# Kernel tuning notes

Measured on AMD Instinct MI355X. Metric: run time of the kernel, lower is better.

The kernel has to match this reference:

```python
import jax, jax.numpy as jnp
import numpy as np

DIM = 1024
HEADS = 16
DIM_HEAD = 64
INNER = HEADS * DIM_HEAD  # 1024
EPS = 1e-5


def setup_inputs() -> dict:
    key = jax.random.key(0)
    ks = jax.random.split(key, 8)
    B, N = 4, 2048
    s = 0.02
    return {
        "query": jax.random.normal(ks[0], (B, N, DIM), jnp.float32),
        "key_": jax.random.normal(ks[1], (B, N, DIM), jnp.float32),
        "value": jax.random.normal(ks[2], (B, N, DIM), jnp.float32),
        "Wq": jax.random.normal(ks[3], (DIM, INNER), jnp.float32) * s,
        "Wk": jax.random.normal(ks[4], (DIM, INNER), jnp.float32) * s,
        "Wv": jax.random.normal(ks[5], (DIM, INNER), jnp.float32) * s,
        "Wo": jax.random.normal(ks[6], (INNER, DIM), jnp.float32) * s,
        "bo": jnp.zeros((DIM,), jnp.float32),
        "gamma": jnp.ones((DIM,), jnp.float32),
        "beta": jnp.zeros((DIM,), jnp.float32),
    }


def reference(query, key_, value, Wq, Wk, Wv, Wo, bo, gamma, beta):
    B, N, _ = query.shape
    scale = DIM_HEAD ** (-0.5)
    # project and split heads: [B, H, N, Dh]
    q = (query @ Wq).reshape(B, N, HEADS, DIM_HEAD).transpose(0, 2, 1, 3)
    k = (key_ @ Wk).reshape(B, N, HEADS, DIM_HEAD).transpose(0, 2, 1, 3)
    v = (value @ Wv).reshape(B, N, HEADS, DIM_HEAD).transpose(0, 2, 1, 3)
    dots = jnp.einsum("bhnd,bhmd->bhnm", q, k) * scale  # [B,H,N,N]
    attn = jax.nn.softmax(dots, axis=-1)
    out = jnp.einsum("bhnm,bhmd->bhnd", attn, v)
    out = out.transpose(0, 2, 1, 3).reshape(B, N, INNER)
    out = out @ Wo + bo  # dropout p=0.0 is identity
    # LayerNorm over last dim
    mu = out.mean(-1, keepdims=True)
    var = ((out - mu) ** 2).mean(-1, keepdims=True)
    normed = (out - mu) * jax.lax.rsqrt(var + EPS) * gamma + beta
    return normed + query
```

## Files before the change

### kernel.cpp

```cpp
#include <hip/hip_runtime.h>
#include <stdint.h>

#define K_DIM 1024
#define B_SZ 4
#define N_SEQ 2048
#define HEADS 16
#define DH 64
#define M_TOT (B_SZ * N_SEQ)

typedef __bf16 bf16x8 __attribute__((ext_vector_type(8)));
typedef __bf16 bf16x4 __attribute__((ext_vector_type(4)));
typedef __bf16 bf16x2 __attribute__((ext_vector_type(2)));
typedef float f32x4 __attribute__((ext_vector_type(4)));
typedef float f32x16 __attribute__((ext_vector_type(16)));

typedef const uint32_t __attribute__((address_space(1))) gas_u32;
typedef uint32_t __attribute__((address_space(3))) las_u32;

#define CE_SCALE 0.1803368801f

__device__ __forceinline__ uint16_t f2bf(float f) {
  uint32_t u = __float_as_uint(f);
  u += 0x7FFFu + ((u >> 16) & 1u);
  return (uint16_t)(u >> 16);
}

__device__ __forceinline__ void gld_lds16(const uint16_t* g, uint16_t* lds) {
  __builtin_amdgcn_global_load_lds((gas_u32*)g, (las_u32*)lds, 16, 0, 0);
}

__device__ __forceinline__ uint32_t pkbf(float a, float b) {
  bf16x2 t;
  t[0] = (__bf16)a;
  t[1] = (__bf16)b;
  return __builtin_bit_cast(uint32_t, t);
}

__device__ __forceinline__ void pswap(uint32_t& a, uint32_t& b) {
  asm("v_permlane32_swap_b32 %0, %1" : "+v"(a), "+v"(b));
}

__global__ __launch_bounds__(256) void conv_bf16_k(const float* __restrict__ s0,
                                                   const float* __restrict__ s1,
                                                   const float* __restrict__ s2,
                                                   uint16_t* __restrict__ dstbase, int n4) {
  const int z = blockIdx.y;
  const float* src = (z == 0) ? s0 : (z == 1) ? s1 : s2;
  uint16_t* dst = dstbase + (size_t)z * M_TOT * K_DIM;
  int i = blockIdx.x * blockDim.x + threadIdx.x;
  if (i < n4) {
    float4 v = ((const float4*)src)[i];
    ushort4 o;
    o.x = f2bf(v.x); o.y = f2bf(v.y); o.z = f2bf(v.z); o.w = f2bf(v.w);
    ((ushort4*)dst)[i] = o;
  }
}

__global__ __launch_bounds__(256) void transpose_conv(const float* __restrict__ s0,
                                                      const float* __restrict__ s1,
                                                      const float* __restrict__ s2,
                                                      const float* __restrict__ s3,
                                                      uint16_t* __restrict__ dstbase) {
  __shared__ float tile[32][33];
  const int z = blockIdx.z;
  const float* src = (z == 0) ? s0 : (z == 1) ? s1 : (z == 2) ? s2 : s3;
  uint16_t* dst = dstbase + (size_t)z * 1024 * 1024;
  const int tx = threadIdx.x, ty = threadIdx.y;
  const int bx = blockIdx.x * 32, by = blockIdx.y * 32;
#pragma unroll
  for (int i = 0; i < 32; i += 8)
    tile[ty + i][tx] = src[(size_t)(by + ty + i) * 1024 + bx + tx];
  __syncthreads();
#pragma unroll
  for (int i = 0; i < 32; i += 8)
    dst[(size_t)(bx + ty + i) * 1024 + by + tx] = f2bf(tile[tx][ty + i]);
}

template <int MODE>
__global__ __launch_bounds__(256, 2) void gemm_bf16(const uint16_t* __restrict__ A,
                                                    const uint16_t* __restrict__ BT,
                                                    void* __restrict__ Cout,
                                                    const float* __restrict__ bias) {
  __shared__ __align__(16) uint16_t As[2][128 * 32];
  __shared__ __align__(16) uint16_t Bs[2][128 * 32];
  const int tid = threadIdx.x;
  const int wave = tid >> 6, lane = tid & 63;
  const int g = lane >> 4, c16 = lane & 15;

  const int bid = blockIdx.x;
  const int xcd = bid & 7;
  const int l = bid >> 3;
  const int z = (MODE == 3) ? (l >> 6) : 0;
  const int r = l & 63;
  const int n0 = (r & 7) * 128;
  const int m0 = (xcd * 8 + (r >> 3)) * 128;

  const int wr = wave >> 1, wc = wave & 1;
  float scale = 1.f;
  if (MODE == 3) {
    A += (size_t)z * M_TOT * K_DIM;
    BT += (size_t)z * 1024 * 1024;
    scale = (z == 0) ? CE_SCALE : 1.f;
  }

  const f32x4 fzero = {0.f, 0.f, 0.f, 0.f};
  f32x4 acc[4][4];
#pragma unroll
  for (int i = 0; i < 4; ++i)
#pragma unroll
    for (int j = 0; j < 4; ++j) acc[i][j] = fzero;

  const int srow = wave * 32 + (lane >> 2);
  const int scol = (((lane & 3) ^ ((srow >> 1) & 3)) * 8);
  const uint16_t* ag0 = A + (size_t)(m0 + srow) * K_DIM + scol;
  const uint16_t* ag1 = A + (size_t)(m0 + srow + 16) * K_DIM + scol;
  const uint16_t* bg0 = BT + (size_t)(n0 + srow) * K_DIM + scol;
  const uint16_t* bg1 = BT + (size_t)(n0 + srow + 16) * K_DIM + scol;
  const int lofa0 = (wave * 32) * 32;
  const int lofa1 = (wave * 32 + 16) * 32;

  const int rk = (c16 >> 1) & 3;

  gld_lds16(ag0, &As[0][lofa0]);
  gld_lds16(ag1, &As[0][lofa1]);
  gld_lds16(bg0, &Bs[0][lofa0]);
  gld_lds16(bg1, &Bs[0][lofa1]);
  __syncthreads();

  int cur = 0;
  for (int kt = 0; kt < K_DIM / 32; ++kt) {
    if (kt + 1 < K_DIM / 32) {
      const int nxt = cur ^ 1;
      gld_lds16(ag0 + (kt + 1) * 32, &As[nxt][lofa0]);
      gld_lds16(ag1 + (kt + 1) * 32, &As[nxt][lofa1]);
      gld_lds16(bg0 + (kt + 1) * 32, &Bs[nxt][lofa0]);
      gld_lds16(bg1 + (kt + 1) * 32, &Bs[nxt][lofa1]);
    }
    bf16x8 avec[4], bvec[4];
#pragma unroll
    for (int i = 0; i < 4; ++i)
      avec[i] = *(const bf16x8*)&As[cur][(wr * 64 + i * 16 + c16) * 32 + ((g ^ rk) << 3)];
#pragma unroll
    for (int j = 0; j < 4; ++j)
      bvec[j] = *(const bf16x8*)&Bs[cur][(wc * 64 + j * 16 + c16) * 32 + ((g ^ rk) << 3)];
#pragma unroll
    for (int i = 0; i < 4; ++i)
#pragma unroll
      for (int j = 0; j < 4; ++j)
        acc[i][j] = __builtin_amdgcn_mfma_f32_16x16x32_bf16(avec[i], bvec[j], acc[i][j], 0, 0, 0);
    __syncthreads();
    cur ^= 1;
  }

#pragma unroll
  for (int i = 0; i < 4; ++i) {
#pragma unroll
    for (int j = 0; j < 4; ++j) {
      const int col = n0 + wc * 64 + j * 16 + c16;
      if (MODE == 3 && z == 2) {
        const int h = col >> 6, d = col & 63;
        const int row0 = m0 + wr * 64 + i * 16 + g * 4;
        const int b = row0 >> 11, n = row0 & 2047;
        ushort4 o;
        o.x = f2bf(acc[i][j][0]); o.y = f2bf(acc[i][j][1]);
        o.z = f2bf(acc[i][j][2]); o.w = f2bf(acc[i][j][3]);
        *(ushort4*)&((uint16_t*)Cout)[(size_t)2 * M_TOT * 1024 +
                                      (((size_t)(b * HEADS + h)) * DH + d) * N_SEQ + n] = o;
      } else {
#pragma unroll
        for (int r2 = 0; r2 < 4; ++r2) {
          const int row = m0 + wr * 64 + i * 16 + g * 4 + r2;
          if (MODE == 3) {
            const int b = row >> 11, n = row & 2047;
            const int h = col >> 6, d = col & 63;
            ((uint16_t*)Cout)[(size_t)z * M_TOT * 1024 +
                              (((size_t)(b * HEADS + h)) * N_SEQ + n) * DH + d] =
                f2bf(acc[i][j][r2] * scale);
          } else {
            ((float*)Cout)[(size_t)row * 1024 + col] = acc[i][j][r2] + bias[col];
          }
        }
      }
    }
  }
}

__global__ __launch_bounds__(256, 2) void attention_k(const uint16_t* __restrict__ qm,
                                                      const uint16_t* __restrict__ km,
                                                      const uint16_t* __restrict__ vtm,
                                                      uint16_t* __restrict__ om) {
  __shared__ __align__(16) uint16_t Ks[2 * 64 * 64];
  __shared__ __align__(16) uint16_t Vs[2 * 64 * 64];
  const int tid = threadIdx.x;
  const int wave = tid >> 6, lane = tid & 63;
  const int lrow = lane & 31;
  const int hi = lane >> 5;

  const int bid = blockIdx.x;
  const int xcd = bid & 7;
  const int l0 = bid >> 3;
  const int bh = xcd * 8 + (l0 & 7);
  const int qblk = l0 >> 3;
  const int b = bh >> 4, h = bh & 15;
  const int q0w = qblk * 256 + wave * 64;

  const uint16_t* qbase = qm + (size_t)bh * N_SEQ * DH;
  const uint16_t* kbase = km + (size_t)bh * N_SEQ * DH;
  const uint16_t* vbase = vtm + (size_t)bh * DH * N_SEQ;

  bf16x8 qf[2][4];
#pragma unroll
  for (int qs = 0; qs < 2; ++qs) {
    const uint16_t* qp = qbase + (size_t)(q0w + qs * 32 + lrow) * DH + hi * 8;
#pragma unroll
    for (int step = 0; step < 4; ++step) qf[qs][step] = *(const bf16x8*)(qp + step * 16);
  }

  int koff[2][4];
  int voff[2][2][2];
#pragma unroll
  for (int ks = 0; ks < 2; ++ks) {
    const int krow = ks * 32 + lrow;
#pragma unroll
    for (int step = 0; step < 4; ++step)
      koff[ks][step] = krow * 64 + ((((step << 1) | hi) ^ (krow & 7)) << 3);
#pragma unroll
    for (int s = 0; s < 2; ++s)
#pragma unroll
      for (int dt = 0; dt < 2; ++dt)
        voff[ks][s][dt] =
            (dt * 32 + lrow) * 64 + ((((ks << 2) | (s << 1) | hi) ^ (lrow & 7)) << 3);
  }

  f32x16 oacc[2][2];
#pragma unroll
  for (int qs = 0; qs < 2; ++qs)
#pragma unroll
    for (int dt = 0; dt < 2; ++dt)
#pragma unroll
      for (int i = 0; i < 16; ++i) oacc[qs][dt][i] = 0.f;
  float l[2] = {0.f, 0.f};

  const int ch = tid & 7;
  const int krow0 = tid >> 3, krow1 = 32 + (tid >> 3);
  const int kdst0 = krow0 * 64 + ((ch ^ (krow0 & 7)) << 3);
  const int kdst1 = krow1 * 64 + ((ch ^ (krow1 & 7)) << 3);

  uint4 kp0, kp1, vp0, vp1;
  kp0 = *(const uint4*)&kbase[(size_t)tid * 8];
  kp1 = *(const uint4*)&kbase[(size_t)(256 + tid) * 8];
  vp0 = *(const uint4*)&vbase[(size_t)krow0 * N_SEQ + ch * 8];
  vp1 = *(const uint4*)&vbase[(size_t)krow1 * N_SEQ + ch * 8];
  *(uint4*)&Ks[kdst0] = kp0;
  *(uint4*)&Ks[kdst1] = kp1;
  *(uint4*)&Vs[kdst0] = vp0;
  *(uint4*)&Vs[kdst1] = vp1;
  __syncthreads();

  for (int t = 0; t < N_SEQ / 64; ++t) {
    const int cur = t & 1;
    if (t < N_SEQ / 64 - 1) {
      const size_t ko = (size_t)(t + 1) * 4096;
      const int vc = (t + 1) * 64;
      kp0 = *(const uint4*)&kbase[ko + (size_t)tid * 8];
      kp1 = *(const uint4*)&kbase[ko + (size_t)(256 + tid) * 8];
      vp0 = *(const uint4*)&vbase[(size_t)krow0 * N_SEQ + vc + ch * 8];
      vp1 = *(const uint4*)&vbase[(size_t)krow1 * N_SEQ + vc + ch * 8];
    }
    const uint16_t* ksp = &Ks[cur * 4096];
    const uint16_t* vsp = &Vs[cur * 4096];

#pragma unroll
    for (int ks = 0; ks < 2; ++ks) {
      bf16x8 kf[4];
#pragma unroll
      for (int step = 0; step < 4; ++step) kf[step] = *(const bf16x8*)&ksp[koff[ks][step]];

      f32x16 z[2];
#pragma unroll
      for (int qs = 0; qs < 2; ++qs)
#pragma unroll
        for (int i = 0; i < 16; ++i) z[qs][i] = 0.f;

      __builtin_amdgcn_s_setprio(1);
#pragma unroll
      for (int step = 0; step < 4; ++step)
        z[0] = __builtin_amdgcn_mfma_f32_32x32x16_bf16(kf[step], qf[0][step], z[0], 0, 0, 0);
#pragma unroll
      for (int step = 0; step < 4; ++step)
        z[1] = __builtin_amdgcn_mfma_f32_32x32x16_bf16(kf[step], qf[1][step], z[1], 0, 0, 0);
      __builtin_amdgcn_s_setprio(0);

      uint32_t pa[2][2][4];
#pragma unroll
      for (int qs = 0; qs < 2; ++qs) {
        float p[16];
#pragma unroll
        for (int r = 0; r < 16; ++r) p[r] = __builtin_amdgcn_exp2f(z[qs][r]);
        l[qs] += (((p[0] + p[1]) + (p[2] + p[3])) + ((p[4] + p[5]) + (p[6] + p[7]))) +
                 (((p[8] + p[9]) + (p[10] + p[11])) + ((p[12] + p[13]) + (p[14] + p[15])));
#pragma unroll
        for (int s = 0; s < 2; ++s) {
          uint32_t w0 = pkbf(p[s * 8 + 0], p[s * 8 + 1]);
          uint32_t w1 = pkbf(p[s * 8 + 2], p[s * 8 + 3]);
          uint32_t w2 = pkbf(p[s * 8 + 4], p[s * 8 + 5]);
          uint32_t w3 = pkbf(p[s * 8 + 6], p[s * 8 + 7]);
          pswap(w0, w2);
          pswap(w1, w3);
          pa[qs][s][0] = w0; pa[qs][s][1] = w1; pa[qs][s][2] = w2; pa[qs][s][3] = w3;
        }
      }

      bf16x8 vf[2][2];
#pragma unroll
      for (int s = 0; s < 2; ++s)
#pragma unroll
        for (int dt = 0; dt < 2; ++dt) vf[s][dt] = *(const bf16x8*)&vsp[voff[ks][s][dt]];

      __builtin_amdgcn_s_setprio(1);
#pragma unroll
      for (int s = 0; s < 2; ++s)
#pragma unroll
        for (int qs = 0; qs < 2; ++qs) {
          uint4 u;
          u.x = pa[qs][s][0]; u.y = pa[qs][s][1]; u.z = pa[qs][s][2]; u.w = pa[qs][s][3];
          const bf16x8 paf = __builtin_bit_cast(bf16x8, u);
          oacc[qs][0] = __builtin_amdgcn_mfma_f32_32x32x16_bf16(paf, vf[s][0], oacc[qs][0], 0, 0, 0);
          oacc[qs][1] = __builtin_amdgcn_mfma_f32_32x32x16_bf16(paf, vf[s][1], oacc[qs][1], 0, 0, 0);
        }
      __builtin_amdgcn_s_setprio(0);
    }

    if (t < N_SEQ / 64 - 1) {
      *(uint4*)&Ks[(cur ^ 1) * 4096 + kdst0] = kp0;
      *(uint4*)&Ks[(cur ^ 1) * 4096 + kdst1] = kp1;
      *(uint4*)&Vs[(cur ^ 1) * 4096 + kdst0] = vp0;
      *(uint4*)&Vs[(cur ^ 1) * 4096 + kdst1] = vp1;
      __syncthreads();
    }
  }

#pragma unroll
  for (int qs = 0; qs < 2; ++qs) l[qs] += __shfl_xor(l[qs], 32);

#pragma unroll
  for (int qs = 0; qs < 2; ++qs) {
#pragma unroll
    for (int r = 0; r < 16; ++r) {
      const int ql = (r & 3) + 8 * (r >> 2) + 4 * hi;
      const float lr = __shfl(l[qs], ql);
      const float inv = 1.f / lr;
      const int row = q0w + qs * 32 + ql;
      const size_t base = ((size_t)b * N_SEQ + row) * 1024 + h * 64;
      om[base + lrow] = f2bf(oacc[qs][0][r] * inv);
      om[base + 32 + lrow] = f2bf(oacc[qs][1][r] * inv);
    }
  }
}

__global__ __launch_bounds__(256) void ln_res_k(const float* __restrict__ proj,
                                                const float* __restrict__ query,
                                                const float* __restrict__ gamma,
                                                const float* __restrict__ beta,
                                                float* __restrict__ out) {
  const int row = blockIdx.x;
  const int tid = threadIdx.x;
  const size_t base = (size_t)row * 1024 + tid * 4;
  float4 v = *(const float4*)(proj + base);
  float s = v.x + v.y + v.z + v.w;
  float s2 = v.x * v.x + v.y * v.y + v.z * v.z + v.w * v.w;
#pragma unroll
  for (int off = 1; off < 64; off <<= 1) {
    s += __shfl_xor(s, off);
    s2 += __shfl_xor(s2, off);
  }
  __shared__ float red[8];
  const int wave = tid >> 6, lane = tid & 63;
  if (lane == 0) { red[wave] = s; red[4 + wave] = s2; }
  __syncthreads();
  s = red[0] + red[1] + red[2] + red[3];
  s2 = red[4] + red[5] + red[6] + red[7];
  const float mu = s * (1.f / 1024.f);
  const float var = fmaxf(s2 * (1.f / 1024.f) - mu * mu, 0.f);
  const float rstd = rsqrtf(var + 1e-5f);
  float4 gq = *(const float4*)(gamma + tid * 4);
  float4 bq = *(const float4*)(beta + tid * 4);
  float4 qq = *(const float4*)(query + base);
  float4 o;
  o.x = (v.x - mu) * rstd * gq.x + bq.x + qq.x;
  o.y = (v.y - mu) * rstd * gq.y + bq.y + qq.y;
  o.z = (v.z - mu) * rstd * gq.z + bq.z + qq.z;
  o.w = (v.w - mu) * rstd * gq.w + bq.w + qq.w;
  *(float4*)(out + base) = o;
}

extern "C" void kernel_launch(void* const* d_in, const int* in_sizes, int n_in,
                              void* d_out, int out_size, void* d_ws, size_t ws_size,
                              hipStream_t stream) {
  (void)in_sizes; (void)n_in; (void)out_size; (void)ws_size;
  const float* query = (const float*)d_in[0];
  const float* key_ = (const float*)d_in[1];
  const float* value = (const float*)d_in[2];
  const float* Wq = (const float*)d_in[3];
  const float* Wk = (const float*)d_in[4];
  const float* Wv = (const float*)d_in[5];
  const float* Wo = (const float*)d_in[6];
  const float* bo = (const float*)d_in[7];
  const float* gamma = (const float*)d_in[8];
  const float* beta = (const float*)d_in[9];
  float* out = (float*)d_out;

  const size_t NELEM = (size_t)M_TOT * 1024;
  uint16_t* wsp = (uint16_t*)d_ws;
  uint16_t* WqT = wsp;
  uint16_t* WoT = WqT + 3 * 1024 * 1024;
  uint16_t* xq = WqT + 4 * 1024 * 1024;
  uint16_t* qb = xq + 3 * NELEM;
  uint16_t* attnO = xq;
  float* proj = (float*)(xq + NELEM);

  const int n4 = (int)(NELEM / 4);
  conv_bf16_k<<<dim3(8192, 3), 256, 0, stream>>>(query, key_, value, xq, n4);

  transpose_conv<<<dim3(32, 32, 4), dim3(32, 8), 0, stream>>>(Wq, Wk, Wv, Wo, WqT);

  gemm_bf16<3><<<1536, 256, 0, stream>>>(xq, WqT, qb, nullptr);

  attention_k<<<512, 256, 0, stream>>>(qb, qb + NELEM, qb + 2 * NELEM, attnO);

  gemm_bf16<1><<<512, 256, 0, stream>>>(attnO, WoT, proj, bo);

  ln_res_k<<<8192, 256, 0, stream>>>(proj, query, gamma, beta, out);
}
```

Measured before the change: 343.6 us.

## Fuse fp32-to-bf16 input conversion into the QKV projection GEMM

Removes the standalone kernel that converted query/key/value to bf16. A new QKV GEMM loads the fp32 activations directly into registers, packs them to bf16 and stores them into shared memory, while weights keep using direct global-to-LDS loads. This avoids a full write and reread of the bf16 activation copies and one kernel launch. In exchange the GEMM reads twice as many bytes for A and does the conversion and LDS stores in its main loop.

New measurement: 356.4 us. 1.04x slower.

```diff
diff --git a/kernel.cpp b/kernel.cpp
--- a/kernel.cpp
+++ b/kernel.cpp
@@ -38,22 +38,6 @@
 
 __device__ __forceinline__ void pswap(uint32_t& a, uint32_t& b) {
   asm("v_permlane32_swap_b32 %0, %1" : "+v"(a), "+v"(b));
-}
-
-__global__ __launch_bounds__(256) void conv_bf16_k(const float* __restrict__ s0,
-                                                   const float* __restrict__ s1,
-                                                   const float* __restrict__ s2,
-                                                   uint16_t* __restrict__ dstbase, int n4) {
-  const int z = blockIdx.y;
-  const float* src = (z == 0) ? s0 : (z == 1) ? s1 : s2;
-  uint16_t* dst = dstbase + (size_t)z * M_TOT * K_DIM;
-  int i = blockIdx.x * blockDim.x + threadIdx.x;
-  if (i < n4) {
-    float4 v = ((const float4*)src)[i];
-    ushort4 o;
-    o.x = f2bf(v.x); o.y = f2bf(v.y); o.z = f2bf(v.z); o.w = f2bf(v.w);
-    ((ushort4*)dst)[i] = o;
-  }
 }
 
 __global__ __launch_bounds__(256) void transpose_conv(const float* __restrict__ s0,
@@ -76,6 +60,133 @@
     dst[(size_t)(bx + ty + i) * 1024 + by + tx] = f2bf(tile[tx][ty + i]);
 }
 
+__global__ __launch_bounds__(256, 2) void gemm_qkv_f32(const float* __restrict__ Aq,
+                                                       const float* __restrict__ Ak,
+                                                       const float* __restrict__ Av,
+                                                       const uint16_t* __restrict__ BT,
+                                                       uint16_t* __restrict__ Cout) {
+  __shared__ __align__(16) uint16_t As[2][128 * 32];
+  __shared__ __align__(16) uint16_t Bs[2][128 * 32];
+  const int tid = threadIdx.x;
+  const int wave = tid >> 6, lane = tid & 63;
+  const int g = lane >> 4, c16 = lane & 15;
+
+  const int bid = blockIdx.x;
+  const int xcd = bid & 7;
+  const int l = bid >> 3;
+  const int z = l >> 6;
+  const int r = l & 63;
+  const int n0 = (r & 7) * 128;
+  const int m0 = (xcd * 8 + (r >> 3)) * 128;
+
+  const int wr = wave >> 1, wc = wave & 1;
+  const float scale = (z == 0) ? CE_SCALE : 1.f;
+  const float* A = (z == 0) ? Aq : (z == 1) ? Ak : Av;
+  BT += (size_t)z * 1024 * 1024;
+
+  const f32x4 fzero = {0.f, 0.f, 0.f, 0.f};
+  f32x4 acc[4][4];
+#pragma unroll
+  for (int i = 0; i < 4; ++i)
+#pragma unroll
+    for (int j = 0; j < 4; ++j) acc[i][j] = fzero;
+
+  const int srow = wave * 32 + (lane >> 2);
+  const int ch4 = lane & 3;
+  const float* ag0 = A + (size_t)(m0 + srow) * K_DIM + ch4 * 8;
+  const float* ag1 = ag0 + (size_t)16 * K_DIM;
+  const int akey = (srow >> 1) & 3;
+  const int adst0 = srow * 32 + ((ch4 ^ akey) << 3);
+  const int adst1 = (srow + 16) * 32 + ((ch4 ^ akey) << 3);
+  const int scol = ((ch4 ^ akey) * 8);
+  const uint16_t* bg0 = BT + (size_t)(n0 + srow) * K_DIM + scol;
+  const uint16_t* bg1 = bg0 + (size_t)16 * K_DIM;
+  const int lofb0 = (wave * 32) * 32;
+  const int lofb1 = (wave * 32 + 16) * 32;
+
+  const int rk = (c16 >> 1) & 3;
+
+  float4 a0a = *(const float4*)(ag0);
+  float4 a0b = *(const float4*)(ag0 + 4);
+  float4 a1a = *(const float4*)(ag1);
+  float4 a1b = *(const float4*)(ag1 + 4);
+  gld_lds16(bg0, &Bs[0][lofb0]);
+  gld_lds16(bg1, &Bs[0][lofb1]);
+  {
+    uint4 w0, w1;
+    w0.x = pkbf(a0a.x, a0a.y); w0.y = pkbf(a0a.z, a0a.w);
+    w0.z = pkbf(a0b.x, a0b.y); w0.w = pkbf(a0b.z, a0b.w);
+    w1.x = pkbf(a1a.x, a1a.y); w1.y = pkbf(a1a.z, a1a.w);
+    w1.z = pkbf(a1b.x, a1b.y); w1.w = pkbf(a1b.z, a1b.w);
+    *(uint4*)&As[0][adst0] = w0;
+    *(uint4*)&As[0][adst1] = w1;
+  }
+  __syncthreads();
+
+  int cur = 0;
+  for (int kt = 0; kt < K_DIM / 32; ++kt) {
+    const int nxt = cur ^ 1;
+    if (kt + 1 < K_DIM / 32) {
+      a0a = *(const float4*)(ag0 + (kt + 1) * 32);
+      a0b = *(const float4*)(ag0 + (kt + 1) * 32 + 4);
+      a1a = *(const float4*)(ag1 + (kt + 1) * 32);
+      a1b = *(const float4*)(ag1 + (kt + 1) * 32 + 4);
+      gld_lds16(bg0 + (kt + 1) * 32, &Bs[nxt][lofb0]);
+      gld_lds16(bg1 + (kt + 1) * 32, &Bs[nxt][lofb1]);
+    }
+    bf16x8 avec[4], bvec[4];
+#pragma unroll
+    for (int i = 0; i < 4; ++i)
+      avec[i] = *(const bf16x8*)&As[cur][(wr * 64 + i * 16 + c16) * 32 + ((g ^ rk) << 3)];
+#pragma unroll
+    for (int j = 0; j < 4; ++j)
+      bvec[j] = *(const bf16x8*)&Bs[cur][(wc * 64 + j * 16 + c16) * 32 + ((g ^ rk) << 3)];
+#pragma unroll
+    for (int i = 0; i < 4; ++i)
+#pragma unroll
+      for (int j = 0; j < 4; ++j)
+        acc[i][j] = __builtin_amdgcn_mfma_f32_16x16x32_bf16(avec[i], bvec[j], acc[i][j], 0, 0, 0);
+    if (kt + 1 < K_DIM / 32) {
+      uint4 w0, w1;
+      w0.x = pkbf(a0a.x, a0a.y); w0.y = pkbf(a0a.z, a0a.w);
+      w0.z = pkbf(a0b.x, a0b.y); w0.w = pkbf(a0b.z, a0b.w);
+      w1.x = pkbf(a1a.x, a1a.y); w1.y = pkbf(a1a.z, a1a.w);
+      w1.z = pkbf(a1b.x, a1b.y); w1.w = pkbf(a1b.z, a1b.w);
+      *(uint4*)&As[nxt][adst0] = w0;
+      *(uint4*)&As[nxt][adst1] = w1;
+    }
+    __syncthreads();
+    cur = nxt;
+  }
+
+#pragma unroll
+  for (int i = 0; i < 4; ++i) {
+#pragma unroll
+    for (int j = 0; j < 4; ++j) {
+      const int col = n0 + wc * 64 + j * 16 + c16;
+      if (z == 2) {
+        const int h = col >> 6, d = col & 63;
+        const int row0 = m0 + wr * 64 + i * 16 + g * 4;
+        const int b = row0 >> 11, n = row0 & 2047;
+        ushort4 o;
+        o.x = f2bf(acc[i][j][0]); o.y = f2bf(acc[i][j][1]);
+        o.z = f2bf(acc[i][j][2]); o.w = f2bf(acc[i][j][3]);
+        *(ushort4*)&Cout[(size_t)2 * M_TOT * 1024 +
+                         (((size_t)(b * HEADS + h)) * DH + d) * N_SEQ + n] = o;
+      } else {
+#pragma unroll
+        for (int r2 = 0; r2 < 4; ++r2) {
+          const int row = m0 + wr * 64 + i * 16 + g * 4 + r2;
+          const int b = row >> 11, n = row & 2047;
+          const int h = col >> 6, d = col & 63;
+          Cout[(size_t)z * M_TOT * 1024 + (((size_t)(b * HEADS + h)) * N_SEQ + n) * DH + d] =
+              f2bf(acc[i][j][r2] * scale);
+        }
+      }
+    }
+  }
+}
+
 template <int MODE>
 __global__ __launch_bounds__(256, 2) void gemm_bf16(const uint16_t* __restrict__ A,
                                                     const uint16_t* __restrict__ BT,
@@ -90,18 +201,11 @@
   const int bid = blockIdx.x;
   const int xcd = bid & 7;
   const int l = bid >> 3;
-  const int z = (MODE == 3) ? (l >> 6) : 0;
   const int r = l & 63;
   const int n0 = (r & 7) * 128;
   const int m0 = (xcd * 8 + (r >> 3)) * 128;
 
   const int wr = wave >> 1, wc = wave & 1;
-  float scale = 1.f;
-  if (MODE == 3) {
-    A += (size_t)z * M_TOT * K_DIM;
-    BT += (size_t)z * 1024 * 1024;
-    scale = (z == 0) ? CE_SCALE : 1.f;
-  }
 
   const f32x4 fzero = {0.f, 0.f, 0.f, 0.f};
   f32x4 acc[4][4];
@@ -157,29 +261,10 @@
 #pragma unroll
     for (int j = 0; j < 4; ++j) {
       const int col = n0 + wc * 64 + j * 16 + c16;
-      if (MODE == 3 && z == 2) {
-        const int h = col >> 6, d = col & 63;
-        const int row0 = m0 + wr * 64 + i * 16 + g * 4;
-        const int b = row0 >> 11, n = row0 & 2047;
-        ushort4 o;
-        o.x = f2bf(acc[i][j][0]); o.y = f2bf(acc[i][j][1]);
-        o.z = f2bf(acc[i][j][2]); o.w = f2bf(acc[i][j][3]);
-        *(ushort4*)&((uint16_t*)Cout)[(size_t)2 * M_TOT * 1024 +
-                                      (((size_t)(b * HEADS + h)) * DH + d) * N_SEQ + n] = o;
-      } else {
-#pragma unroll
-        for (int r2 = 0; r2 < 4; ++r2) {
-          const int row = m0 + wr * 64 + i * 16 + g * 4 + r2;
-          if (MODE == 3) {
-            const int b = row >> 11, n = row & 2047;
-            const int h = col >> 6, d = col & 63;
-            ((uint16_t*)Cout)[(size_t)z * M_TOT * 1024 +
-                              (((size_t)(b * HEADS + h)) * N_SEQ + n) * DH + d] =
-                f2bf(acc[i][j][r2] * scale);
-          } else {
-            ((float*)Cout)[(size_t)row * 1024 + col] = acc[i][j][r2] + bias[col];
-          }
-        }
+#pragma unroll
+      for (int r2 = 0; r2 < 4; ++r2) {
+        const int row = m0 + wr * 64 + i * 16 + g * 4 + r2;
+        ((float*)Cout)[(size_t)row * 1024 + col] = acc[i][j][r2] + bias[col];
       }
     }
   }
@@ -419,12 +504,9 @@
   uint16_t* attnO = xq;
   float* proj = (float*)(xq + NELEM);
 
-  const int n4 = (int)(NELEM / 4);
-  conv_bf16_k<<<dim3(8192, 3), 256, 0, stream>>>(query, key_, value, xq, n4);
-
   transpose_conv<<<dim3(32, 32, 4), dim3(32, 8), 0, stream>>>(Wq, Wk, Wv, Wo, WqT);
 
-  gemm_bf16<3><<<1536, 256, 0, stream>>>(xq, WqT, qb, nullptr);
+  gemm_qkv_f32<<<1536, 256, 0, stream>>>(query, key_, value, WqT, qb);
 
   attention_k<<<512, 256, 0, stream>>>(qb, qb + NELEM, qb + 2 * NELEM, attnO);
 
```
